# Kernel tuning notes

Hardware: AMD Instinct MI355X
Metric: run time of the kernel (lower is better)

Reference implementation:

```python
import jax, jax.numpy as jnp
import numpy as np

D_MODEL = 512
LR = 0.01
CLIP = 0.5
B, T = 8, 4096


def setup_inputs() -> dict:
    key = jax.random.key(0)
    k1, k2, k3 = jax.random.split(key, 3)
    x = jax.random.normal(k1, (B, T, D_MODEL), dtype=jnp.float32)
    W_current = jnp.zeros((D_MODEL, D_MODEL), dtype=jnp.float32)
    W_base = jax.random.normal(k2, (D_MODEL, D_MODEL), dtype=jnp.float32) * 0.02
    gate_w = jax.random.normal(k3, (D_MODEL, D_MODEL), dtype=jnp.float32) * (1.0 / np.sqrt(D_MODEL))
    gate_b = jnp.zeros((D_MODEL,), dtype=jnp.float32)
    return {"x": x, "W_current": W_current, "W_base": W_base, "gate_w": gate_w, "gate_b": gate_b}


def reference(x, W_current, W_base, gate_w, gate_b):
    # x: [B, T, D]; W_current, W_base, gate_w: [D, D]; gate_b: [D]
    def step(W_c, x_t):  # x_t: [B, D]
        W = W_base + W_c
        mem_read = x_t @ W.T                       # [B, D]
        gate = jax.nn.sigmoid(x_t @ gate_w.T + gate_b)
        out_t = gate * mem_read
        # fast-weight update (torch.no_grad -> stop_gradient)
        surprise_avg = jax.lax.stop_gradient((x_t - mem_read).mean(axis=0))
        x_avg = jax.lax.stop_gradient(x_t.mean(axis=0))
        dW = jnp.outer(surprise_avg, x_avg)        # [D, D]
        n = jnp.linalg.norm(dW)
        dW = dW * jnp.where(n > CLIP, CLIP / n, 1.0)
        W_new = W_c + LR * dW
        return W_new, out_t

    xs = jnp.swapaxes(x, 0, 1)                     # [T, B, D]
    W_final, outs = jax.lax.scan(step, W_current, xs)
    out = jnp.swapaxes(outs, 0, 1)                 # [B, T, D]
    return out, W_final
```

## Files before the change

kernel.cpp:

```cpp
#include <hip/hip_runtime.h>
#include <math.h>

#define BB 8
#define TT 4096
#define DD 512
constexpr float LRF = 0.01f;

#define OFF_A  0
#define OFF_CU 2097152
#define OFF_G  4194304
#define OFF_P  5242880
#define OFF_BV 5373952
#define OFF_W  5406720
#define OFF_WS 5668864
#define OFF_S  9863168

__global__ void tm_mean(const float* __restrict__ x, float* __restrict__ a) {
    int idx = blockIdx.x * 256 + threadIdx.x;
    float s = 0.f;
#pragma unroll
    for (int b = 0; b < BB; ++b) s += x[b * (TT * DD) + idx];
    a[idx] = s * 0.125f;
}

__global__ void tm_init(const float* __restrict__ wb, const float* __restrict__ wc,
                        float* __restrict__ W, float* __restrict__ Wsnap) {
    int idx = blockIdx.x * 256 + threadIdx.x;
    float v = wb[idx] + wc[idx];
    W[idx] = v;
    Wsnap[idx] = v;
}

__global__ __launch_bounds__(256) void tm_gram(const float* __restrict__ a, float* __restrict__ G) {
    __shared__ float sl[64 * 65];
    __shared__ float tl[64 * 65];
    int bid = blockIdx.x;
    int p = bid >> 4, ts = (bid >> 2) & 3, tt = bid & 3;
    int tid = threadIdx.x;
    int c0 = (tid & 15) * 4, r0 = (tid >> 4) * 4;
    float acc[4][4] = {};
    for (int kt = 0; kt < 8; ++kt) {
        if (kt) __syncthreads();
        for (int l = tid; l < 64 * 16; l += 256) {
            int r = l >> 4, c4 = (l & 15) * 4;
            float4 v = *(const float4*)&a[(p * 256 + ts * 64 + r) * DD + kt * 64 + c4];
            sl[r * 65 + c4] = v.x; sl[r * 65 + c4 + 1] = v.y;
            sl[r * 65 + c4 + 2] = v.z; sl[r * 65 + c4 + 3] = v.w;
            float4 u = *(const float4*)&a[(p * 256 + tt * 64 + r) * DD + kt * 64 + c4];
            tl[r * 65 + c4] = u.x; tl[r * 65 + c4 + 1] = u.y;
            tl[r * 65 + c4 + 2] = u.z; tl[r * 65 + c4 + 3] = u.w;
        }
        __syncthreads();
        for (int kk = 0; kk < 64; ++kk) {
            float as[4], at[4];
#pragma unroll
            for (int q = 0; q < 4; ++q) { as[q] = sl[(r0 + q) * 65 + kk]; at[q] = tl[(c0 + q) * 65 + kk]; }
#pragma unroll
            for (int q = 0; q < 4; ++q)
#pragma unroll
                for (int w2 = 0; w2 < 4; ++w2) acc[q][w2] += as[q] * at[w2];
        }
    }
#pragma unroll
    for (int q = 0; q < 4; ++q) {
        float4 v = make_float4(acc[q][0], acc[q][1], acc[q][2], acc[q][3]);
        *(float4*)&G[p * 65536 + (ts * 64 + r0 + q) * 256 + tt * 64 + c0] = v;
    }
}

__global__ __launch_bounds__(256) void tm_P(const float* __restrict__ a, const float* __restrict__ W,
                                            float* __restrict__ P, int p) {
    __shared__ float al[64 * 65];
    __shared__ float wl[64 * 65];
    int bid = blockIdx.x;
    int bt = bid & 3, bi = bid >> 2;
    int tid = threadIdx.x;
    int c0 = (tid & 15) * 4, r0 = (tid >> 4) * 4;
    float acc[4][4] = {};
    for (int kt = 0; kt < 8; ++kt) {
        if (kt) __syncthreads();
        for (int l = tid; l < 64 * 16; l += 256) {
            int r = l >> 4, c4 = (l & 15) * 4;
            float4 v = *(const float4*)&a[(p * 256 + bt * 64 + r) * DD + kt * 64 + c4];
            al[r * 65 + c4] = v.x; al[r * 65 + c4 + 1] = v.y;
            al[r * 65 + c4 + 2] = v.z; al[r * 65 + c4 + 3] = v.w;
            float4 u = *(const float4*)&W[(bi * 64 + r) * DD + kt * 64 + c4];
            wl[r * 65 + c4] = u.x; wl[r * 65 + c4 + 1] = u.y;
            wl[r * 65 + c4 + 2] = u.z; wl[r * 65 + c4 + 3] = u.w;
        }
        __syncthreads();
        for (int kk = 0; kk < 64; ++kk) {
            float af[4], bf[4];
#pragma unroll
            for (int q = 0; q < 4; ++q) { af[q] = al[(r0 + q) * 65 + kk]; bf[q] = wl[(c0 + q) * 65 + kk]; }
#pragma unroll
            for (int q = 0; q < 4; ++q)
#pragma unroll
                for (int w2 = 0; w2 < 4; ++w2) acc[q][w2] += af[q] * bf[w2];
        }
    }
#pragma unroll
    for (int q = 0; q < 4; ++q) {
        float4 av = *(const float4*)&a[(p * 256 + bt * 64 + r0 + q) * DD + bi * 64 + c0];
        float4 v = make_float4(av.x - acc[q][0], av.y - acc[q][1],
                               av.z - acc[q][2], av.w - acc[q][3]);
        *(float4*)&P[(bt * 64 + r0 + q) * DD + bi * 64 + c0] = v;
    }
}

__global__ __launch_bounds__(256) void tm_corr(const float* __restrict__ P, const float* __restrict__ G,
                                               const float* __restrict__ CU, float* __restrict__ bv,
                                               int p, int j) {
    __shared__ float gsl[64 * 65];
    __shared__ float cul[64 * 65];
    int bd = blockIdx.x;
    int tid = threadIdx.x;
    int c0 = (tid & 15) * 4, r0 = (tid >> 4) * 4;
    const float* Gp = G + p * 65536;
    float acc[4][4] = {};
    for (int kb = 0; kb < j * 64; kb += 64) {
        if (kb) __syncthreads();
        for (int l = tid; l < 64 * 16; l += 256) {
            int r = l >> 4, c4 = (l & 15) * 4;
            float4 v = *(const float4*)&Gp[(kb + r) * 256 + j * 64 + c4];
            gsl[r * 65 + c4] = v.x; gsl[r * 65 + c4 + 1] = v.y;
            gsl[r * 65 + c4 + 2] = v.z; gsl[r * 65 + c4 + 3] = v.w;
            float4 u = *(const float4*)&CU[(p * 256 + kb + r) * DD + bd * 64 + c4];
            cul[r * 65 + c4] = u.x; cul[r * 65 + c4 + 1] = u.y;
            cul[r * 65 + c4 + 2] = u.z; cul[r * 65 + c4 + 3] = u.w;
        }
        __syncthreads();
        for (int kk = 0; kk < 64; ++kk) {
            float gf[4], cf[4];
#pragma unroll
            for (int q = 0; q < 4; ++q) { gf[q] = gsl[kk * 65 + r0 + q]; cf[q] = cul[kk * 65 + c0 + q]; }
#pragma unroll
            for (int q = 0; q < 4; ++q)
#pragma unroll
                for (int w2 = 0; w2 < 4; ++w2) acc[q][w2] += gf[q] * cf[w2];
        }
    }
#pragma unroll
    for (int q = 0; q < 4; ++q) {
        float4 pv = *(const float4*)&P[(j * 64 + r0 + q) * DD + bd * 64 + c0];
        float4 v = make_float4(pv.x - LRF * acc[q][0], pv.y - LRF * acc[q][1],
                               pv.z - LRF * acc[q][2], pv.w - LRF * acc[q][3]);
        *(float4*)&bv[(r0 + q) * DD + bd * 64 + c0] = v;
    }
}

__global__ __launch_bounds__(256) void tm_scan(const float* __restrict__ bv, const float* __restrict__ G,
                                               float* __restrict__ cu, int kchunk) {
    __shared__ float gl[64 * 64];
    __shared__ float part[2][4];
    int tid = threadIdx.x;
    int wid = tid >> 6, lane = tid & 63;
    int p = kchunk >> 2, j = kchunk & 3;
    const float* Gp = G + p * 65536;
    for (int l = tid; l < 64 * 16; l += 256) {
        int r = l >> 4, c4 = (l & 15) * 4;
        float4 v = *(const float4*)&Gp[(j * 64 + r) * 256 + j * 64 + c4];
        *(float4*)&gl[r * 64 + c4] = v;
    }
    float acc0[64], acc1[64];
#pragma unroll
    for (int t = 0; t < 64; ++t) {
        acc0[t] = bv[t * DD + tid];
        acc1[t] = bv[t * DD + tid + 256];
    }
    __syncthreads();
    float* cup = cu + (p * 256 + j * 64) * DD;
#pragma unroll
    for (int s = 0; s < 64; ++s) {
        float u0 = acc0[s], u1 = acc1[s];
        float v = u0 * u0 + u1 * u1;
#pragma unroll
        for (int off = 32; off > 0; off >>= 1) v += __shfl_xor(v, off, 64);
        if (lane == 0) part[s & 1][wid] = v;
        __syncthreads();
        float n2u = part[s & 1][0] + part[s & 1][1] + part[s & 1][2] + part[s & 1][3];
        float n2 = n2u * gl[s * 64 + s];
        float cs = (n2 > 0.25f) ? 0.5f * rsqrtf(n2) : 1.0f;
        cup[s * DD + tid] = cs * u0;
        cup[s * DD + tid + 256] = cs * u1;
        float w0 = (LRF * cs) * u0, w1 = (LRF * cs) * u1;
        int t0 = s + 1;
#pragma unroll
        for (; t0 < 64 && (t0 & 3); ++t0) {
            float g = gl[s * 64 + t0];
            acc0[t0] -= g * w0; acc1[t0] -= g * w1;
        }
#pragma unroll
        for (; t0 < 64; t0 += 4) {
            float4 g4 = *(const float4*)&gl[s * 64 + t0];
            acc0[t0]     -= g4.x * w0; acc1[t0]     -= g4.x * w1;
            acc0[t0 + 1] -= g4.y * w0; acc1[t0 + 1] -= g4.y * w1;
            acc0[t0 + 2] -= g4.z * w0; acc1[t0 + 2] -= g4.z * w1;
            acc0[t0 + 3] -= g4.w * w0; acc1[t0 + 3] -= g4.w * w1;
        }
    }
}

__global__ void tm_wupd(const float* __restrict__ a, const float* __restrict__ cu,
                        float* __restrict__ W, float* __restrict__ Wsnap,
                        const float* __restrict__ wb, float* __restrict__ outW,
                        int p, int snap_p, int is_final) {
    int idx = blockIdx.x * 256 + threadIdx.x;
    int i = idx >> 9, jj = idx & 511;
    const float* cb = cu + p * 256 * DD + i;
    const float* ab = a + p * 256 * DD + jj;
    float s = 0.f;
#pragma unroll 8
    for (int r = 0; r < 256; ++r) s += cb[r * DD] * ab[r * DD];
    float w = W[idx] + LRF * s;
    W[idx] = w;
    if (snap_p >= 0) Wsnap[snap_p * DD * DD + idx] = w;
    if (is_final) outW[idx] = w - wb[idx];
}


__global__ __launch_bounds__(256) void tm_mem(const float* __restrict__ x, const float* __restrict__ Wsnap,
                                              float* __restrict__ out) {
    __shared__ float al[64 * 65];
    __shared__ float bl[64 * 65];
    int bid = blockIdx.x;
    int p = bid >> 8, rem = bid & 255, rt = rem >> 3, it = rem & 7;
    int tid = threadIdx.x;
    int c0 = (tid & 15) * 4, r0 = (tid >> 4) * 4;
    const float* Wp = Wsnap + p * DD * DD;
    float acc[4][4] = {};
    for (int kt = 0; kt < 8; ++kt) {
        if (kt) __syncthreads();
        for (int l = tid; l < 64 * 16; l += 256) {
            int r = l >> 4, c4 = (l & 15) * 4;
            int rloc = rt * 64 + r;
            int grow = ((rloc >> 8) * TT) + p * 256 + (rloc & 255);
            float4 v = *(const float4*)&x[grow * DD + kt * 64 + c4];
            al[r * 65 + c4] = v.x; al[r * 65 + c4 + 1] = v.y;
            al[r * 65 + c4 + 2] = v.z; al[r * 65 + c4 + 3] = v.w;
            float4 u = *(const float4*)&Wp[(it * 64 + r) * DD + kt * 64 + c4];
            bl[r * 65 + c4] = u.x; bl[r * 65 + c4 + 1] = u.y;
            bl[r * 65 + c4 + 2] = u.z; bl[r * 65 + c4 + 3] = u.w;
        }
        __syncthreads();
        for (int kk = 0; kk < 64; ++kk) {
            float af[4], bf[4];
#pragma unroll
            for (int q = 0; q < 4; ++q) { af[q] = al[(r0 + q) * 65 + kk]; bf[q] = bl[(c0 + q) * 65 + kk]; }
#pragma unroll
            for (int q = 0; q < 4; ++q)
#pragma unroll
                for (int w2 = 0; w2 < 4; ++w2) acc[q][w2] += af[q] * bf[w2];
        }
    }
#pragma unroll
    for (int q = 0; q < 4; ++q) {
        int rloc = rt * 64 + r0 + q;
        int grow = ((rloc >> 8) * TT) + p * 256 + (rloc & 255);
        float4 v = make_float4(acc[q][0], acc[q][1], acc[q][2], acc[q][3]);
        *(float4*)&out[grow * DD + it * 64 + c0] = v;
    }
}

__global__ __launch_bounds__(256) void tm_score(const float* __restrict__ x, const float* __restrict__ a,
                                                float* __restrict__ S) {
    __shared__ float al[64 * 65];
    __shared__ float bl[64 * 65];
    int bid = blockIdx.x;
    int st = bid & 3, rt = (bid >> 2) & 31, p = bid >> 7;
    int tid = threadIdx.x;
    int c0 = (tid & 15) * 4, r0 = (tid >> 4) * 4;
    float acc[4][4] = {};
    for (int kt = 0; kt < 8; ++kt) {
        if (kt) __syncthreads();
        for (int l = tid; l < 64 * 16; l += 256) {
            int r = l >> 4, c4 = (l & 15) * 4;
            int rloc = rt * 64 + r;
            int grow = ((rloc >> 8) * TT) + p * 256 + (rloc & 255);
            float4 v = *(const float4*)&x[grow * DD + kt * 64 + c4];
            al[r * 65 + c4] = v.x; al[r * 65 + c4 + 1] = v.y;
            al[r * 65 + c4 + 2] = v.z; al[r * 65 + c4 + 3] = v.w;
            float4 u = *(const float4*)&a[(p * 256 + st * 64 + r) * DD + kt * 64 + c4];
            bl[r * 65 + c4] = u.x; bl[r * 65 + c4 + 1] = u.y;
            bl[r * 65 + c4 + 2] = u.z; bl[r * 65 + c4 + 3] = u.w;
        }
        __syncthreads();
        for (int kk = 0; kk < 64; ++kk) {
            float af[4], bf[4];
#pragma unroll
            for (int q = 0; q < 4; ++q) { af[q] = al[(r0 + q) * 65 + kk]; bf[q] = bl[(c0 + q) * 65 + kk]; }
#pragma unroll
            for (int q = 0; q < 4; ++q)
#pragma unroll
                for (int w2 = 0; w2 < 4; ++w2) acc[q][w2] += af[q] * bf[w2];
        }
    }
#pragma unroll
    for (int q = 0; q < 4; ++q) {
        int rloc = rt * 64 + r0 + q;
        float4 v = make_float4(acc[q][0], acc[q][1], acc[q][2], acc[q][3]);
        *(float4*)&S[(p * 2048 + rloc) * 256 + st * 64 + c0] = v;
    }
}

__global__ __launch_bounds__(256) void tm_apply(const float* __restrict__ S, const float* __restrict__ cu,
                                                float* __restrict__ out) {
    __shared__ float al[64 * 65];
    __shared__ float bl[64 * 65];
    int bid = blockIdx.x;
    int it = bid & 7, rt = (bid >> 3) & 31, p = bid >> 8;
    int tid = threadIdx.x;
    int c0 = (tid & 15) * 4, r0 = (tid >> 4) * 4;
    float acc[4][4] = {};
    for (int kt = 0; kt < 4; ++kt) {
        if (kt) __syncthreads();
        for (int l = tid; l < 64 * 16; l += 256) {
            int r = l >> 4, c4 = (l & 15) * 4;
            int rloc = rt * 64 + r;
            int tq = rloc & 255;
            float4 v = *(const float4*)&S[(p * 2048 + rloc) * 256 + kt * 64 + c4];
            int sb = kt * 64 + c4;
            al[r * 65 + c4]     = (sb + 0 < tq) ? v.x : 0.f;
            al[r * 65 + c4 + 1] = (sb + 1 < tq) ? v.y : 0.f;
            al[r * 65 + c4 + 2] = (sb + 2 < tq) ? v.z : 0.f;
            al[r * 65 + c4 + 3] = (sb + 3 < tq) ? v.w : 0.f;
            float4 u = *(const float4*)&cu[(p * 256 + kt * 64 + r) * DD + it * 64 + c4];
            bl[r * 65 + c4] = u.x; bl[r * 65 + c4 + 1] = u.y;
            bl[r * 65 + c4 + 2] = u.z; bl[r * 65 + c4 + 3] = u.w;
        }
        __syncthreads();
        for (int kk = 0; kk < 64; ++kk) {
            float af[4], bf[4];
#pragma unroll
            for (int q = 0; q < 4; ++q) { af[q] = al[(r0 + q) * 65 + kk]; bf[q] = bl[kk * 65 + c0 + q]; }
#pragma unroll
            for (int q = 0; q < 4; ++q)
#pragma unroll
                for (int w2 = 0; w2 < 4; ++w2) acc[q][w2] += af[q] * bf[w2];
        }
    }
#pragma unroll
    for (int q = 0; q < 4; ++q) {
        int rloc = rt * 64 + r0 + q;
        int grow = ((rloc >> 8) * TT) + p * 256 + (rloc & 255);
        float4 cur = *(float4*)&out[grow * DD + it * 64 + c0];
        cur.x += LRF * acc[q][0]; cur.y += LRF * acc[q][1];
        cur.z += LRF * acc[q][2]; cur.w += LRF * acc[q][3];
        *(float4*)&out[grow * DD + it * 64 + c0] = cur;
    }
}

__global__ __launch_bounds__(256) void tm_gate(const float* __restrict__ x, const float* __restrict__ gw,
                                               const float* __restrict__ gb, float* __restrict__ out) {
    __shared__ float al[64 * 65];
    __shared__ float bl[64 * 65];
    int bid = blockIdx.x;
    int it = bid & 7, rt = bid >> 3;
    int tid = threadIdx.x;
    int c0 = (tid & 15) * 4, r0 = (tid >> 4) * 4;
    float acc[4][4] = {};
    for (int kt = 0; kt < 8; ++kt) {
        if (kt) __syncthreads();
        for (int l = tid; l < 64 * 16; l += 256) {
            int r = l >> 4, c4 = (l & 15) * 4;
            int grow = rt * 64 + r;
            float4 v = *(const float4*)&x[grow * DD + kt * 64 + c4];
            al[r * 65 + c4] = v.x; al[r * 65 + c4 + 1] = v.y;
            al[r * 65 + c4 + 2] = v.z; al[r * 65 + c4 + 3] = v.w;
            float4 u = *(const float4*)&gw[(it * 64 + r) * DD + kt * 64 + c4];
            bl[r * 65 + c4] = u.x; bl[r * 65 + c4 + 1] = u.y;
            bl[r * 65 + c4 + 2] = u.z; bl[r * 65 + c4 + 3] = u.w;
        }
        __syncthreads();
        for (int kk = 0; kk < 64; ++kk) {
            float af[4], bf[4];
#pragma unroll
            for (int q = 0; q < 4; ++q) { af[q] = al[(r0 + q) * 65 + kk]; bf[q] = bl[(c0 + q) * 65 + kk]; }
#pragma unroll
            for (int q = 0; q < 4; ++q)
#pragma unroll
                for (int w2 = 0; w2 < 4; ++w2) acc[q][w2] += af[q] * bf[w2];
        }
    }
#pragma unroll
    for (int q = 0; q < 4; ++q) {
        int grow = rt * 64 + r0 + q;
        float4 cur = *(float4*)&out[grow * DD + it * 64 + c0];
        float z0 = acc[q][0] + gb[it * 64 + c0 + 0];
        float z1 = acc[q][1] + gb[it * 64 + c0 + 1];
        float z2 = acc[q][2] + gb[it * 64 + c0 + 2];
        float z3 = acc[q][3] + gb[it * 64 + c0 + 3];
        cur.x *= 1.f / (1.f + expf(-z0));
        cur.y *= 1.f / (1.f + expf(-z1));
        cur.z *= 1.f / (1.f + expf(-z2));
        cur.w *= 1.f / (1.f + expf(-z3));
        *(float4*)&out[grow * DD + it * 64 + c0] = cur;
    }
}

extern "C" void kernel_launch(void* const* d_in, const int* in_sizes, int n_in,
                              void* d_out, int out_size, void* d_ws, size_t ws_size,
                              hipStream_t stream) {
    const float* x   = (const float*)d_in[0];
    const float* Wc0 = (const float*)d_in[1];
    const float* Wb  = (const float*)d_in[2];
    const float* gw  = (const float*)d_in[3];
    const float* gb  = (const float*)d_in[4];
    float* out  = (float*)d_out;
    float* outW = out + BB * TT * DD;

    float* ws = (float*)d_ws;
    float* A  = ws + OFF_A;
    float* CU = ws + OFF_CU;
    float* G  = ws + OFF_G;
    float* P  = ws + OFF_P;
    float* BV = ws + OFF_BV;
    float* W  = ws + OFF_W;
    float* WS = ws + OFF_WS;
    float* S  = ws + OFF_S;

    tm_mean<<<(TT * DD) / 256, 256, 0, stream>>>(x, A);
    tm_init<<<(DD * DD) / 256, 256, 0, stream>>>(Wb, Wc0, W, WS);
    tm_gram<<<256, 256, 0, stream>>>(A, G);
    tm_P<<<32, 256, 0, stream>>>(A, W, P, 0);

    for (int p = 0; p < 16; ++p) {
        for (int j = 0; j < 4; ++j) {
            tm_corr<<<8, 256, 0, stream>>>(P, G, CU, BV, p, j);
            tm_scan<<<1, 256, 0, stream>>>(BV, G, CU, p * 4 + j);
        }
        if (p < 15) {
            tm_wupd<<<(DD * DD) / 256, 256, 0, stream>>>(A, CU, W, WS, Wb, outW, p, p + 1, 0);
            tm_P<<<32, 256, 0, stream>>>(A, W, P, p + 1);
        }
    }
    tm_wupd<<<(DD * DD) / 256, 256, 0, stream>>>(A, CU, W, WS, Wb, outW, 15, -1, 1);

    tm_mem<<<16 * 256, 256, 0, stream>>>(x, WS, out);
    tm_score<<<16 * 128, 256, 0, stream>>>(x, A, S);
    tm_apply<<<16 * 256, 256, 0, stream>>>(S, CU, out);
    tm_gate<<<512 * 8, 256, 0, stream>>>(x, gw, gb, out);
}
```

Measured before the change: 8.468 ms.

## Fuse sequential scan into persistent kernel with grid barriers and overlapped matmuls

Replaces the roughly 150 small kernel launches of the chunked recurrence with one persistent 256-block kernel that uses an atomic-counter grid barrier between phases. The independent mem, score and apply matmuls are spread across the idle blocks during the serial corr and scan steps, so they overlap with the critical path instead of running afterwards. This removes launch overhead and fills the idle GPU during the sequential part. The cost is a spin barrier that requires all 256 blocks to be co-resident, plus barrier latency at every step.

```diff
diff --git a/kernel.cpp b/kernel.cpp
--- a/kernel.cpp
+++ b/kernel.cpp
@@ -14,85 +14,78 @@
 #define OFF_W  5406720
 #define OFF_WS 5668864
 #define OFF_S  9863168
-
-__global__ void tm_mean(const float* __restrict__ x, float* __restrict__ a) {
-    int idx = blockIdx.x * 256 + threadIdx.x;
-    float s = 0.f;
-#pragma unroll
-    for (int b = 0; b < BB; ++b) s += x[b * (TT * DD) + idx];
-    a[idx] = s * 0.125f;
-}
-
-__global__ void tm_init(const float* __restrict__ wb, const float* __restrict__ wc,
-                        float* __restrict__ W, float* __restrict__ Wsnap) {
-    int idx = blockIdx.x * 256 + threadIdx.x;
-    float v = wb[idx] + wc[idx];
-    W[idx] = v;
-    Wsnap[idx] = v;
-}
-
-__global__ __launch_bounds__(256) void tm_gram(const float* __restrict__ a, float* __restrict__ G) {
-    __shared__ float sl[64 * 65];
-    __shared__ float tl[64 * 65];
-    int bid = blockIdx.x;
-    int p = bid >> 4, ts = (bid >> 2) & 3, tt = bid & 3;
-    int tid = threadIdx.x;
-    int c0 = (tid & 15) * 4, r0 = (tid >> 4) * 4;
+#define OFF_BAR 18251776
+
+__device__ __forceinline__ void gbar(unsigned int* bar) {
+    __syncthreads();
+    if (threadIdx.x == 0) {
+        __threadfence();
+        unsigned int ticket = atomicAdd(bar, 1u);
+        unsigned int target = (ticket & ~255u) + 256u;
+        while (__hip_atomic_load(bar, __ATOMIC_RELAXED, __HIP_MEMORY_SCOPE_AGENT) < target)
+            __builtin_amdgcn_s_sleep(2);
+        __threadfence();
+    }
+    __syncthreads();
+}
+
+__device__ __forceinline__ void mm_stage(const float* ga, const float* gbm,
+                                         float* L0, float* L1, int tid) {
+    for (int l = tid; l < 64 * 16; l += 256) {
+        int r = l >> 4, c4 = (l & 15) * 4;
+        float4 v = *(const float4*)&ga[r * DD + c4];
+        L0[r * 65 + c4] = v.x; L0[r * 65 + c4 + 1] = v.y;
+        L0[r * 65 + c4 + 2] = v.z; L0[r * 65 + c4 + 3] = v.w;
+        float4 u = *(const float4*)&gbm[r * DD + c4];
+        L1[r * 65 + c4] = u.x; L1[r * 65 + c4 + 1] = u.y;
+        L1[r * 65 + c4 + 2] = u.z; L1[r * 65 + c4 + 3] = u.w;
+    }
+}
+
+__device__ __forceinline__ void mm_tile(const float* ga, const float* gbm,
+                                        float* L0, float* L1, int tid, int r0, int c0,
+                                        float acc[4][4]) {
+    for (int kt = 0; kt < 8; ++kt) {
+        __syncthreads();
+        mm_stage(ga + kt * 64, gbm + kt * 64, L0, L1, tid);
+        __syncthreads();
+        for (int kk = 0; kk < 64; ++kk) {
+            float af[4], bf[4];
+#pragma unroll
+            for (int q = 0; q < 4; ++q) { af[q] = L0[(r0 + q) * 65 + kk]; bf[q] = L1[(c0 + q) * 65 + kk]; }
+#pragma unroll
+            for (int q = 0; q < 4; ++q)
+#pragma unroll
+                for (int w2 = 0; w2 < 4; ++w2) acc[q][w2] += af[q] * bf[w2];
+        }
+    }
+}
+
+__device__ __forceinline__ void apply_tile(const float* S, const float* CU, float* out,
+                                           int t_, float* L0, float* L1, int tid, int r0, int c0) {
+    int it = t_ & 7, rt = (t_ >> 3) & 31, p = t_ >> 8;
     float acc[4][4] = {};
-    for (int kt = 0; kt < 8; ++kt) {
-        if (kt) __syncthreads();
+    for (int kt = 0; kt < 4; ++kt) {
+        __syncthreads();
         for (int l = tid; l < 64 * 16; l += 256) {
             int r = l >> 4, c4 = (l & 15) * 4;
-            float4 v = *(const float4*)&a[(p * 256 + ts * 64 + r) * DD + kt * 64 + c4];
-            sl[r * 65 + c4] = v.x; sl[r * 65 + c4 + 1] = v.y;
-            sl[r * 65 + c4 + 2] = v.z; sl[r * 65 + c4 + 3] = v.w;
-            float4 u = *(const float4*)&a[(p * 256 + tt * 64 + r) * DD + kt * 64 + c4];
-            tl[r * 65 + c4] = u.x; tl[r * 65 + c4 + 1] = u.y;
-            tl[r * 65 + c4 + 2] = u.z; tl[r * 65 + c4 + 3] = u.w;
-        }
-        __syncthreads();
-        for (int kk = 0; kk < 64; ++kk) {
-            float as[4], at[4];
-#pragma unroll
-            for (int q = 0; q < 4; ++q) { as[q] = sl[(r0 + q) * 65 + kk]; at[q] = tl[(c0 + q) * 65 + kk]; }
-#pragma unroll
-            for (int q = 0; q < 4; ++q)
-#pragma unroll
-                for (int w2 = 0; w2 < 4; ++w2) acc[q][w2] += as[q] * at[w2];
-        }
-    }
-#pragma unroll
-    for (int q = 0; q < 4; ++q) {
-        float4 v = make_float4(acc[q][0], acc[q][1], acc[q][2], acc[q][3]);
-        *(float4*)&G[p * 65536 + (ts * 64 + r0 + q) * 256 + tt * 64 + c0] = v;
-    }
-}
-
-__global__ __launch_bounds__(256) void tm_P(const float* __restrict__ a, const float* __restrict__ W,
-                                            float* __restrict__ P, int p) {
-    __shared__ float al[64 * 65];
-    __shared__ float wl[64 * 65];
-    int bid = blockIdx.x;
-    int bt = bid & 3, bi = bid >> 2;
-    int tid = threadIdx.x;
-    int c0 = (tid & 15) * 4, r0 = (tid >> 4) * 4;
-    float acc[4][4] = {};
-    for (int kt = 0; kt < 8; ++kt) {
-        if (kt) __syncthreads();
-        for (int l = tid; l < 64 * 16; l += 256) {
-            int r = l >> 4, c4 = (l & 15) * 4;
-            float4 v = *(const float4*)&a[(p * 256 + bt * 64 + r) * DD + kt * 64 + c4];
-            al[r * 65 + c4] = v.x; al[r * 65 + c4 + 1] = v.y;
-            al[r * 65 + c4 + 2] = v.z; al[r * 65 + c4 + 3] = v.w;
-            float4 u = *(const float4*)&W[(bi * 64 + r) * DD + kt * 64 + c4];
-            wl[r * 65 + c4] = u.x; wl[r * 65 + c4 + 1] = u.y;
-            wl[r * 65 + c4 + 2] = u.z; wl[r * 65 + c4 + 3] = u.w;
+            int rloc = rt * 64 + r;
+            int tq = rloc & 255;
+            float4 v = *(const float4*)&S[(p * 2048 + rloc) * 256 + kt * 64 + c4];
+            int sb = kt * 64 + c4;
+            L0[r * 65 + c4]     = (sb + 0 < tq) ? v.x : 0.f;
+            L0[r * 65 + c4 + 1] = (sb + 1 < tq) ? v.y : 0.f;
+            L0[r * 65 + c4 + 2] = (sb + 2 < tq) ? v.z : 0.f;
+            L0[r * 65 + c4 + 3] = (sb + 3 < tq) ? v.w : 0.f;
+            float4 u = *(const float4*)&CU[(p * 256 + kt * 64 + r) * DD + it * 64 + c4];
+            L1[r * 65 + c4] = u.x; L1[r * 65 + c4 + 1] = u.y;
+            L1[r * 65 + c4 + 2] = u.z; L1[r * 65 + c4 + 3] = u.w;
         }
         __syncthreads();
         for (int kk = 0; kk < 64; ++kk) {
             float af[4], bf[4];
 #pragma unroll
-            for (int q = 0; q < 4; ++q) { af[q] = al[(r0 + q) * 65 + kk]; bf[q] = wl[(c0 + q) * 65 + kk]; }
+            for (int q = 0; q < 4; ++q) { af[q] = L0[(r0 + q) * 65 + kk]; bf[q] = L1[kk * 65 + c0 + q]; }
 #pragma unroll
             for (int q = 0; q < 4; ++q)
 #pragma unroll
@@ -101,59 +94,19 @@
     }
 #pragma unroll
     for (int q = 0; q < 4; ++q) {
-        float4 av = *(const float4*)&a[(p * 256 + bt * 64 + r0 + q) * DD + bi * 64 + c0];
-        float4 v = make_float4(av.x - acc[q][0], av.y - acc[q][1],
-                               av.z - acc[q][2], av.w - acc[q][3]);
-        *(float4*)&P[(bt * 64 + r0 + q) * DD + bi * 64 + c0] = v;
-    }
-}
-
-__global__ __launch_bounds__(256) void tm_corr(const float* __restrict__ P, const float* __restrict__ G,
-                                               const float* __restrict__ CU, float* __restrict__ bv,
-                                               int p, int j) {
-    __shared__ float gsl[64 * 65];
-    __shared__ float cul[64 * 65];
-    int bd = blockIdx.x;
-    int tid = threadIdx.x;
-    int c0 = (tid & 15) * 4, r0 = (tid >> 4) * 4;
-    const float* Gp = G + p * 65536;
-    float acc[4][4] = {};
-    for (int kb = 0; kb < j * 64; kb += 64) {
-        if (kb) __syncthreads();
-        for (int l = tid; l < 64 * 16; l += 256) {
-            int r = l >> 4, c4 = (l & 15) * 4;
-            float4 v = *(const float4*)&Gp[(kb + r) * 256 + j * 64 + c4];
-            gsl[r * 65 + c4] = v.x; gsl[r * 65 + c4 + 1] = v.y;
-            gsl[r * 65 + c4 + 2] = v.z; gsl[r * 65 + c4 + 3] = v.w;
-            float4 u = *(const float4*)&CU[(p * 256 + kb + r) * DD + bd * 64 + c4];
-            cul[r * 65 + c4] = u.x; cul[r * 65 + c4 + 1] = u.y;
-            cul[r * 65 + c4 + 2] = u.z; cul[r * 65 + c4 + 3] = u.w;
-        }
-        __syncthreads();
-        for (int kk = 0; kk < 64; ++kk) {
-            float gf[4], cf[4];
-#pragma unroll
-            for (int q = 0; q < 4; ++q) { gf[q] = gsl[kk * 65 + r0 + q]; cf[q] = cul[kk * 65 + c0 + q]; }
-#pragma unroll
-            for (int q = 0; q < 4; ++q)
-#pragma unroll
-                for (int w2 = 0; w2 < 4; ++w2) acc[q][w2] += gf[q] * cf[w2];
-        }
-    }
-#pragma unroll
-    for (int q = 0; q < 4; ++q) {
-        float4 pv = *(const float4*)&P[(j * 64 + r0 + q) * DD + bd * 64 + c0];
-        float4 v = make_float4(pv.x - LRF * acc[q][0], pv.y - LRF * acc[q][1],
-                               pv.z - LRF * acc[q][2], pv.w - LRF * acc[q][3]);
-        *(float4*)&bv[(r0 + q) * DD + bd * 64 + c0] = v;
-    }
-}
-
-__global__ __launch_bounds__(256) void tm_scan(const float* __restrict__ bv, const float* __restrict__ G,
-                                               float* __restrict__ cu, int kchunk) {
-    __shared__ float gl[64 * 64];
-    __shared__ float part[2][4];
-    int tid = threadIdx.x;
+        int rloc = rt * 64 + r0 + q;
+        int grow = ((rloc >> 8) * TT) + p * 256 + (rloc & 255);
+        float4 cur = *(float4*)&out[grow * DD + it * 64 + c0];
+        cur.x += LRF * acc[q][0]; cur.y += LRF * acc[q][1];
+        cur.z += LRF * acc[q][2]; cur.w += LRF * acc[q][3];
+        *(float4*)&out[grow * DD + it * 64 + c0] = cur;
+    }
+}
+
+__device__ void scan_role(const float* BV, const float* G, float* CU, int kchunk,
+                          float* lds, int tid) {
+    float* gl = lds;
+    float* part = lds + 4096;
     int wid = tid >> 6, lane = tid & 63;
     int p = kchunk >> 2, j = kchunk & 3;
     const float* Gp = G + p * 65536;
@@ -165,20 +118,21 @@
     float acc0[64], acc1[64];
 #pragma unroll
     for (int t = 0; t < 64; ++t) {
-        acc0[t] = bv[t * DD + tid];
-        acc1[t] = bv[t * DD + tid + 256];
+        acc0[t] = BV[t * DD + tid];
+        acc1[t] = BV[t * DD + tid + 256];
     }
     __syncthreads();
-    float* cup = cu + (p * 256 + j * 64) * DD;
+    float* cup = CU + (p * 256 + j * 64) * DD;
 #pragma unroll
     for (int s = 0; s < 64; ++s) {
         float u0 = acc0[s], u1 = acc1[s];
         float v = u0 * u0 + u1 * u1;
 #pragma unroll
         for (int off = 32; off > 0; off >>= 1) v += __shfl_xor(v, off, 64);
-        if (lane == 0) part[s & 1][wid] = v;
-        __syncthreads();
-        float n2u = part[s & 1][0] + part[s & 1][1] + part[s & 1][2] + part[s & 1][3];
+        if (lane == 0) part[(s & 1) * 4 + wid] = v;
+        __syncthreads();
+        float n2u = part[(s & 1) * 4 + 0] + part[(s & 1) * 4 + 1]
+                  + part[(s & 1) * 4 + 2] + part[(s & 1) * 4 + 3];
         float n2 = n2u * gl[s * 64 + s];
         float cs = (n2 > 0.25f) ? 0.5f * rsqrtf(n2) : 1.0f;
         cup[s * DD + tid] = cs * u0;
@@ -201,152 +155,161 @@
     }
 }
 
-__global__ void tm_wupd(const float* __restrict__ a, const float* __restrict__ cu,
-                        float* __restrict__ W, float* __restrict__ Wsnap,
-                        const float* __restrict__ wb, float* __restrict__ outW,
-                        int p, int snap_p, int is_final) {
-    int idx = blockIdx.x * 256 + threadIdx.x;
-    int i = idx >> 9, jj = idx & 511;
-    const float* cb = cu + p * 256 * DD + i;
-    const float* ab = a + p * 256 * DD + jj;
-    float s = 0.f;
+__global__ __launch_bounds__(256) void tm_seq(
+    const float* __restrict__ x, const float* __restrict__ Wc0, const float* __restrict__ Wb,
+    float* A, float* CU, float* G, float* P, float* BV, float* W, float* WS, float* S,
+    float* out, float* outW, unsigned int* bar)
+{
+    const int bid = blockIdx.x;
+    const int tid = threadIdx.x;
+    const int c0 = (tid & 15) * 4, r0 = (tid >> 4) * 4;
+
+    __shared__ float lds[2 * 64 * 65 + 16];
+    float* L0 = lds;
+    float* L1 = lds + 64 * 65;
+
+    for (int it = 0; it < 32; ++it) {
+        int idx = (bid * 32 + it) * 256 + tid;
+        float s = 0.f;
+#pragma unroll
+        for (int b = 0; b < BB; ++b) s += x[b * (TT * DD) + idx];
+        A[idx] = s * 0.125f;
+    }
+    for (int it = 0; it < 4; ++it) {
+        int idx = (bid * 4 + it) * 256 + tid;
+        float v = Wb[idx] + Wc0[idx];
+        W[idx] = v; WS[idx] = v;
+    }
+    gbar(bar);
+
+    {
+        int p = bid >> 4, ts = (bid >> 2) & 3, ttl = bid & 3;
+        float acc[4][4] = {};
+        mm_tile(A + (p * 256 + ts * 64) * DD, A + (p * 256 + ttl * 64) * DD,
+                L0, L1, tid, r0, c0, acc);
+#pragma unroll
+        for (int q = 0; q < 4; ++q)
+            *(float4*)&G[p * 65536 + (ts * 64 + r0 + q) * 256 + ttl * 64 + c0] =
+                make_float4(acc[q][0], acc[q][1], acc[q][2], acc[q][3]);
+    }
+    if (bid < 32) {
+        int bt = bid & 3, bi = bid >> 2;
+        float acc[4][4] = {};
+        mm_tile(A + bt * 64 * DD, W + bi * 64 * DD, L0, L1, tid, r0, c0, acc);
+#pragma unroll
+        for (int q = 0; q < 4; ++q) {
+            float4 av = *(const float4*)&A[(bt * 64 + r0 + q) * DD + bi * 64 + c0];
+            *(float4*)&P[(bt * 64 + r0 + q) * DD + bi * 64 + c0] =
+                make_float4(av.x - acc[q][0], av.y - acc[q][1], av.z - acc[q][2], av.w - acc[q][3]);
+        }
+    }
+    gbar(bar);
+
+    for (int p = 0; p < 16; ++p) {
+        for (int j = 0; j < 4; ++j) {
+            if (bid < 8) {
+                const float* Gp = G + p * 65536;
+                int bd = bid;
+                float acc[4][4] = {};
+                for (int kb = 0; kb < j * 64; kb += 64) {
+                    __syncthreads();
+                    for (int l = tid; l < 64 * 16; l += 256) {
+                        int r = l >> 4, c4 = (l & 15) * 4;
+                        float4 v = *(const float4*)&Gp[(kb + r) * 256 + j * 64 + c4];
+                        L0[r * 65 + c4] = v.x; L0[r * 65 + c4 + 1] = v.y;
+                        L0[r * 65 + c4 + 2] = v.z; L0[r * 65 + c4 + 3] = v.w;
+                        float4 u = *(const float4*)&CU[(p * 256 + kb + r) * DD + bd * 64 + c4];
+                        L1[r * 65 + c4] = u.x; L1[r * 65 + c4 + 1] = u.y;
+                        L1[r * 65 + c4 + 2] = u.z; L1[r * 65 + c4 + 3] = u.w;
+                    }
+                    __syncthreads();
+                    for (int kk = 0; kk < 64; ++kk) {
+                        float gf[4], cf[4];
+#pragma unroll
+                        for (int q = 0; q < 4; ++q) { gf[q] = L0[kk * 65 + r0 + q]; cf[q] = L1[kk * 65 + c0 + q]; }
+#pragma unroll
+                        for (int q = 0; q < 4; ++q)
+#pragma unroll
+                            for (int w2 = 0; w2 < 4; ++w2) acc[q][w2] += gf[q] * cf[w2];
+                    }
+                }
+#pragma unroll
+                for (int q = 0; q < 4; ++q) {
+                    float4 pv = *(const float4*)&P[(j * 64 + r0 + q) * DD + bd * 64 + c0];
+                    *(float4*)&BV[(r0 + q) * DD + bd * 64 + c0] =
+                        make_float4(pv.x - LRF * acc[q][0], pv.y - LRF * acc[q][1],
+                                    pv.z - LRF * acc[q][2], pv.w - LRF * acc[q][3]);
+                }
+            } else if (bid < 72 && p > 0) {
+                int t_ = (p - 1) * 256 + j * 64 + (bid - 8);
+                apply_tile(S, CU, out, t_, L0, L1, tid, r0, c0);
+            }
+            gbar(bar);
+
+            int k = p * 4 + j;
+            if (bid == 0) {
+                scan_role(BV, G, CU, k, lds, tid);
+            } else if (bid < 33) {
+                int t_ = k * 32 + (bid - 1);
+                int st = t_ & 3, rt = (t_ >> 2) & 31, ps = t_ >> 7;
+                int growbase = (rt >> 2) * TT + ps * 256 + (rt & 3) * 64;
+                float acc[4][4] = {};
+                mm_tile(x + growbase * DD, A + (ps * 256 + st * 64) * DD,
+                        L0, L1, tid, r0, c0, acc);
+#pragma unroll
+                for (int q = 0; q < 4; ++q)
+                    *(float4*)&S[(ps * 2048 + rt * 64 + r0 + q) * 256 + st * 64 + c0] =
+                        make_float4(acc[q][0], acc[q][1], acc[q][2], acc[q][3]);
+            } else if (bid < 97) {
+                int t_ = k * 64 + (bid - 33);
+                int pm = t_ >> 8, rem = t_ & 255, rt = rem >> 3, itile = rem & 7;
+                int growbase = (rt >> 2) * TT + pm * 256 + (rt & 3) * 64;
+                float acc[4][4] = {};
+                mm_tile(x + growbase * DD, WS + pm * DD * DD + itile * 64 * DD,
+                        L0, L1, tid, r0, c0, acc);
+#pragma unroll
+                for (int q = 0; q < 4; ++q)
+                    *(float4*)&out[(growbase + r0 + q) * DD + itile * 64 + c0] =
+                        make_float4(acc[q][0], acc[q][1], acc[q][2], acc[q][3]);
+            }
+            gbar(bar);
+        }
+
+        for (int it = 0; it < 4; ++it) {
+            int idx = (bid * 4 + it) * 256 + tid;
+            int i = idx >> 9, jj = idx & 511;
+            const float* cb = CU + p * 256 * DD + i;
+            const float* ab = A + p * 256 * DD + jj;
+            float s = 0.f;
 #pragma unroll 8
-    for (int r = 0; r < 256; ++r) s += cb[r * DD] * ab[r * DD];
-    float w = W[idx] + LRF * s;
-    W[idx] = w;
-    if (snap_p >= 0) Wsnap[snap_p * DD * DD + idx] = w;
-    if (is_final) outW[idx] = w - wb[idx];
-}
-
-
-__global__ __launch_bounds__(256) void tm_mem(const float* __restrict__ x, const float* __restrict__ Wsnap,
-                                              float* __restrict__ out) {
-    __shared__ float al[64 * 65];
-    __shared__ float bl[64 * 65];
-    int bid = blockIdx.x;
-    int p = bid >> 8, rem = bid & 255, rt = rem >> 3, it = rem & 7;
-    int tid = threadIdx.x;
-    int c0 = (tid & 15) * 4, r0 = (tid >> 4) * 4;
-    const float* Wp = Wsnap + p * DD * DD;
-    float acc[4][4] = {};
-    for (int kt = 0; kt < 8; ++kt) {
-        if (kt) __syncthreads();
-        for (int l = tid; l < 64 * 16; l += 256) {
-            int r = l >> 4, c4 = (l & 15) * 4;
-            int rloc = rt * 64 + r;
-            int grow = ((rloc >> 8) * TT) + p * 256 + (rloc & 255);
-            float4 v = *(const float4*)&x[grow * DD + kt * 64 + c4];
-            al[r * 65 + c4] = v.x; al[r * 65 + c4 + 1] = v.y;
-            al[r * 65 + c4 + 2] = v.z; al[r * 65 + c4 + 3] = v.w;
-            float4 u = *(const float4*)&Wp[(it * 64 + r) * DD + kt * 64 + c4];
-            bl[r * 65 + c4] = u.x; bl[r * 65 + c4 + 1] = u.y;
-            bl[r * 65 + c4 + 2] = u.z; bl[r * 65 + c4 + 3] = u.w;
-        }
-        __syncthreads();
-        for (int kk = 0; kk < 64; ++kk) {
-            float af[4], bf[4];
-#pragma unroll
-            for (int q = 0; q < 4; ++q) { af[q] = al[(r0 + q) * 65 + kk]; bf[q] = bl[(c0 + q) * 65 + kk]; }
-#pragma unroll
-            for (int q = 0; q < 4; ++q)
-#pragma unroll
-                for (int w2 = 0; w2 < 4; ++w2) acc[q][w2] += af[q] * bf[w2];
-        }
-    }
-#pragma unroll
-    for (int q = 0; q < 4; ++q) {
-        int rloc = rt * 64 + r0 + q;
-        int grow = ((rloc >> 8) * TT) + p * 256 + (rloc & 255);
-        float4 v = make_float4(acc[q][0], acc[q][1], acc[q][2], acc[q][3]);
-        *(float4*)&out[grow * DD + it * 64 + c0] = v;
-    }
-}
-
-__global__ __launch_bounds__(256) void tm_score(const float* __restrict__ x, const float* __restrict__ a,
-                                                float* __restrict__ S) {
-    __shared__ float al[64 * 65];
-    __shared__ float bl[64 * 65];
-    int bid = blockIdx.x;
-    int st = bid & 3, rt = (bid >> 2) & 31, p = bid >> 7;
-    int tid = threadIdx.x;
-    int c0 = (tid & 15) * 4, r0 = (tid >> 4) * 4;
-    float acc[4][4] = {};
-    for (int kt = 0; kt < 8; ++kt) {
-        if (kt) __syncthreads();
-        for (int l = tid; l < 64 * 16; l += 256) {
-            int r = l >> 4, c4 = (l & 15) * 4;
-            int rloc = rt * 64 + r;
-            int grow = ((rloc >> 8) * TT) + p * 256 + (rloc & 255);
-            float4 v = *(const float4*)&x[grow * DD + kt * 64 + c4];
-            al[r * 65 + c4] = v.x; al[r * 65 + c4 + 1] = v.y;
-            al[r * 65 + c4 + 2] = v.z; al[r * 65 + c4 + 3] = v.w;
-            float4 u = *(const float4*)&a[(p * 256 + st * 64 + r) * DD + kt * 64 + c4];
-            bl[r * 65 + c4] = u.x; bl[r * 65 + c4 + 1] = u.y;
-            bl[r * 65 + c4 + 2] = u.z; bl[r * 65 + c4 + 3] = u.w;
-        }
-        __syncthreads();
-        for (int kk = 0; kk < 64; ++kk) {
-            float af[4], bf[4];
-#pragma unroll
-            for (int q = 0; q < 4; ++q) { af[q] = al[(r0 + q) * 65 + kk]; bf[q] = bl[(c0 + q) * 65 + kk]; }
-#pragma unroll
-            for (int q = 0; q < 4; ++q)
-#pragma unroll
-                for (int w2 = 0; w2 < 4; ++w2) acc[q][w2] += af[q] * bf[w2];
-        }
-    }
-#pragma unroll
-    for (int q = 0; q < 4; ++q) {
-        int rloc = rt * 64 + r0 + q;
-        float4 v = make_float4(acc[q][0], acc[q][1], acc[q][2], acc[q][3]);
-        *(float4*)&S[(p * 2048 + rloc) * 256 + st * 64 + c0] = v;
-    }
-}
-
-__global__ __launch_bounds__(256) void tm_apply(const float* __restrict__ S, const float* __restrict__ cu,
-                                                float* __restrict__ out) {
-    __shared__ float al[64 * 65];
-    __shared__ float bl[64 * 65];
-    int bid = blockIdx.x;
-    int it = bid & 7, rt = (bid >> 3) & 31, p = bid >> 8;
-    int tid = threadIdx.x;
-    int c0 = (tid & 15) * 4, r0 = (tid >> 4) * 4;
-    float acc[4][4] = {};
-    for (int kt = 0; kt < 4; ++kt) {
-        if (kt) __syncthreads();
-        for (int l = tid; l < 64 * 16; l += 256) {
-            int r = l >> 4, c4 = (l & 15) * 4;
-            int rloc = rt * 64 + r;
-            int tq = rloc & 255;
-            float4 v = *(const float4*)&S[(p * 2048 + rloc) * 256 + kt * 64 + c4];
-            int sb = kt * 64 + c4;
-            al[r * 65 + c4]     = (sb + 0 < tq) ? v.x : 0.f;
-            al[r * 65 + c4 + 1] = (sb + 1 < tq) ? v.y : 0.f;
-            al[r * 65 + c4 + 2] = (sb + 2 < tq) ? v.z : 0.f;
-            al[r * 65 + c4 + 3] = (sb + 3 < tq) ? v.w : 0.f;
-            float4 u = *(const float4*)&cu[(p * 256 + kt * 64 + r) * DD + it * 64 + c4];
-            bl[r * 65 + c4] = u.x; bl[r * 65 + c4 + 1] = u.y;
-            bl[r * 65 + c4 + 2] = u.z; bl[r * 65 + c4 + 3] = u.w;
-        }
-        __syncthreads();
-        for (int kk = 0; kk < 64; ++kk) {
-            float af[4], bf[4];
-#pragma unroll
-            for (int q = 0; q < 4; ++q) { af[q] = al[(r0 + q) * 65 + kk]; bf[q] = bl[kk * 65 + c0 + q]; }
-#pragma unroll
-            for (int q = 0; q < 4; ++q)
-#pragma unroll
-                for (int w2 = 0; w2 < 4; ++w2) acc[q][w2] += af[q] * bf[w2];
-        }
-    }
-#pragma unroll
-    for (int q = 0; q < 4; ++q) {
-        int rloc = rt * 64 + r0 + q;
-        int grow = ((rloc >> 8) * TT) + p * 256 + (rloc & 255);
-        float4 cur = *(float4*)&out[grow * DD + it * 64 + c0];
-        cur.x += LRF * acc[q][0]; cur.y += LRF * acc[q][1];
-        cur.z += LRF * acc[q][2]; cur.w += LRF * acc[q][3];
-        *(float4*)&out[grow * DD + it * 64 + c0] = cur;
+            for (int r = 0; r < 256; ++r) s += cb[r * DD] * ab[r * DD];
+            float w = W[idx] + LRF * s;
+            W[idx] = w;
+            if (p < 15) WS[(p + 1) * DD * DD + idx] = w;
+            else outW[idx] = w - Wb[idx];
+        }
+        gbar(bar);
+
+        if (p < 15) {
+            if (bid < 32) {
+                int bt = bid & 3, bi = bid >> 2;
+                float acc[4][4] = {};
+                mm_tile(A + ((p + 1) * 256 + bt * 64) * DD, W + bi * 64 * DD,
+                        L0, L1, tid, r0, c0, acc);
+#pragma unroll
+                for (int q = 0; q < 4; ++q) {
+                    float4 av = *(const float4*)&A[((p + 1) * 256 + bt * 64 + r0 + q) * DD + bi * 64 + c0];
+                    *(float4*)&P[(bt * 64 + r0 + q) * DD + bi * 64 + c0] =
+                        make_float4(av.x - acc[q][0], av.y - acc[q][1], av.z - acc[q][2], av.w - acc[q][3]);
+                }
+            }
+            gbar(bar);
+        }
+    }
+
+    {
+        int t_ = 15 * 256 + bid;
+        apply_tile(S, CU, out, t_, L0, L1, tid, r0, c0);
     }
 }
 
@@ -418,26 +381,10 @@
     float* W  = ws + OFF_W;
     float* WS = ws + OFF_WS;
     float* S  = ws + OFF_S;
-
-    tm_mean<<<(TT * DD) / 256, 256, 0, stream>>>(x, A);
-    tm_init<<<(DD * DD) / 256, 256, 0, stream>>>(Wb, Wc0, W, WS);
-    tm_gram<<<256, 256, 0, stream>>>(A, G);
-    tm_P<<<32, 256, 0, stream>>>(A, W, P, 0);
-
-    for (int p = 0; p < 16; ++p) {
-        for (int j = 0; j < 4; ++j) {
-            tm_corr<<<8, 256, 0, stream>>>(P, G, CU, BV, p, j);
-            tm_scan<<<1, 256, 0, stream>>>(BV, G, CU, p * 4 + j);
-        }
-        if (p < 15) {
-            tm_wupd<<<(DD * DD) / 256, 256, 0, stream>>>(A, CU, W, WS, Wb, outW, p, p + 1, 0);
-            tm_P<<<32, 256, 0, stream>>>(A, W, P, p + 1);
-        }
-    }
-    tm_wupd<<<(DD * DD) / 256, 256, 0, stream>>>(A, CU, W, WS, Wb, outW, 15, -1, 1);
-
-    tm_mem<<<16 * 256, 256, 0, stream>>>(x, WS, out);
-    tm_score<<<16 * 128, 256, 0, stream>>>(x, A, S);
-    tm_apply<<<16 * 256, 256, 0, stream>>>(S, CU, out);
+    unsigned int* bar = (unsigned int*)(ws + OFF_BAR);
+
+    hipMemsetAsync((void*)bar, 0, 256, stream);
+
+    tm_seq<<<256, 256, 0, stream>>>(x, Wc0, Wb, A, CU, G, P, BV, W, WS, S, out, outW, bar);
     tm_gate<<<512 * 8, 256, 0, stream>>>(x, gw, gb, out);
 }
```

Measured after the change: 17.34 ms. +104.7%, slower.
